# Kernel optimization log

Hardware: AMD Instinct MI355X
Metric: run time of the kernel (lower is better)

Reference implementation:

```python
import jax, jax.numpy as jnp
import numpy as np

SEQ, BATCH, D_MODEL = 1536, 2, 1024
N_HEAD, D_HEAD, N_ROLL = 16, 64, 3
SCALE = 1.0 / float(np.sqrt(D_HEAD))
EPS_DENOM = 1e-5
EPS_LN = 1e-5


def _dpfp(x, n_roll=N_ROLL):
    # relu feature map: cat(relu(x), relu(-x)), then roll-multiply expansion
    x = jnp.concatenate([jax.nn.relu(x), jax.nn.relu(-x)], axis=-1)  # [S,B,N,2D]
    return jnp.concatenate(
        [x * jnp.roll(x, shift=i, axis=-1) for i in range(1, n_roll + 1)], axis=-1
    )  # [S,B,N,2D*n_roll]


def setup_inputs() -> dict:
    key = jax.random.key(0)
    k_h, k_q, k_kv, k_o = jax.random.split(key, 4)
    std = 1.0 / float(np.sqrt(D_MODEL))
    h = jax.random.normal(k_h, (SEQ, BATCH, D_MODEL), jnp.float32)
    Wq = jax.random.normal(k_q, (N_HEAD * D_HEAD, D_MODEL), jnp.float32) * std
    Wkv = jax.random.normal(k_kv, (2 * N_HEAD * D_HEAD, D_MODEL), jnp.float32) * std
    Wo = jax.random.normal(k_o, (D_MODEL, N_HEAD * D_HEAD), jnp.float32) * std
    ln_gamma = jnp.ones((D_MODEL,), jnp.float32)
    ln_beta = jnp.zeros((D_MODEL,), jnp.float32)
    # Transformer-XL causal mask: triu(ones(qlen, klen), 1)[:, :, None] -> dim 3
    attn_mask = jnp.triu(jnp.ones((SEQ, SEQ), bool), k=1)[:, :, None]
    return {"h": h, "Wq": Wq, "Wkv": Wkv, "Wo": Wo,
            "ln_gamma": ln_gamma, "ln_beta": ln_beta, "attn_mask": attn_mask}


def reference(h, Wq, Wkv, Wo, ln_gamma, ln_beta, attn_mask):
    S, B, _ = h.shape
    # projections (no mems, post-lnorm, eval mode -> dropout identity)
    q = (h @ Wq.T).reshape(S, B, N_HEAD, D_HEAD)
    k, v = jnp.split(h @ Wkv.T, 2, axis=-1)
    k = k.reshape(S, B, N_HEAD, D_HEAD)
    v = v.reshape(S, B, N_HEAD, D_HEAD)
    # DPFP feature maps -> feature dim 2*D_HEAD*N_ROLL
    q = _dpfp(q)
    k = _dpfp(k)
    # kernelized scores [S,S,B,N]
    score = jnp.einsum('ibnd,jbnd->ijbn', q, k) * SCALE
    # 3-D mask [qlen,klen,1] -> broadcast over (b via size-1) and heads
    score = jnp.where(attn_mask[:, :, :, None], 0.0, score)
    # sum-normalization over keys (axis 1 = j)
    denom = jnp.sum(score, axis=1, keepdims=True) + EPS_DENOM
    prob = score / denom
    attn_vec = jnp.einsum('ijbn,jbnd->ibnd', prob, v).reshape(S, B, N_HEAD * D_HEAD)
    attn_out = attn_vec @ Wo.T
    # post-layernorm residual
    x = h + attn_out
    mean = jnp.mean(x, axis=-1, keepdims=True)
    var = jnp.var(x, axis=-1, keepdims=True)
    return ln_gamma * (x - mean) / jnp.sqrt(var + EPS_LN) + ln_beta
```

## Files before the change

### kernel.cpp

```cpp
#include <hip/hip_runtime.h>
#include <hip/hip_bf16.h>

#define S_LEN 1536
#define BATCH 2
#define DMODEL 1024
#define NHEAD 16
#define DHEAD 64
#define FDIM 384
#define CHUNK 64
#define NCHUNK 24
#define ROWS (S_LEN*BATCH)
#define SCALE_F 0.125f
#define EPS_D 1e-5f
#define EPS_LN 1e-5f

typedef unsigned short u16;
typedef __attribute__((ext_vector_type(8))) __bf16 bf16x8;
typedef __attribute__((ext_vector_type(8))) unsigned short ushort8;
typedef __attribute__((ext_vector_type(4))) float f32x4;

static __device__ __forceinline__ float bf2f(u16 a) {
  return __uint_as_float(((unsigned)a) << 16);
}
static __device__ __forceinline__ u16 f2bf(float x) {
  unsigned u = __float_as_uint(x);
  unsigned r = (u + 0x7FFFu + ((u >> 16) & 1u)) >> 16;
  return (u16)r;
}
static __device__ __forceinline__ void gload_lds16(const void* g, void* l) {
  __builtin_amdgcn_global_load_lds(
      (const __attribute__((address_space(1))) void*)g,
      (__attribute__((address_space(3))) void*)l, 16, 0, 0);
}
#define MFMA(a, b, c) __builtin_amdgcn_mfma_f32_16x16x32_bf16(a, b, c, 0, 0, 0)


__global__ __launch_bounds__(256) void cvt_bf16(
    const float* __restrict__ in, u16* __restrict__ out, int n4) {
  int i = blockIdx.x * 256 + threadIdx.x;
  if (i < n4) {
    float4 v = ((const float4*)in)[i];
    ushort4 o = {f2bf(v.x), f2bf(v.y), f2bf(v.z), f2bf(v.w)};
    ((ushort4*)out)[i] = o;
  }
}

__global__ __launch_bounds__(256) void gemm_bf16_mfma(
    const u16* __restrict__ A, const u16* __restrict__ B,
    float* __restrict__ C, int M, int N, int K) {
  __shared__ u16 As[128 * 32];
  __shared__ u16 Bs[128 * 32];
  const int t = threadIdx.x;
  const int l = t & 63, w = t >> 6;
  const int m0 = blockIdx.y * 128, n0 = blockIdx.x * 128;
  const int wm = (w >> 1) * 64, wn = (w & 1) * 64;

  f32x4 acc[4][4];
#pragma unroll
  for (int i = 0; i < 4; ++i)
#pragma unroll
    for (int j = 0; j < 4; ++j) acc[i][j] = (f32x4)0.f;

  const size_t Kb = (size_t)K * 2;
  const int o_lo = w * 1024 + l * 16;
  const int o_hi = 4096 + w * 1024 + l * 16;
  const int r_lo = o_lo >> 6, kb_lo = o_lo & 63;
  const int r_hi = o_hi >> 6, kb_hi = o_hi & 63;

  const char* Ap0 = (const char*)A + (size_t)(m0 + r_lo) * Kb + kb_lo;
  const char* Ap1 = (const char*)A + (size_t)(m0 + r_hi) * Kb + kb_hi;
  const char* Bp0 = (const char*)B + (size_t)(n0 + r_lo) * Kb + kb_lo;
  const char* Bp1 = (const char*)B + (size_t)(n0 + r_hi) * Kb + kb_hi;
  u16* AsB0 = As + (w * 1024) / 2;
  u16* AsB1 = As + (4096 + w * 1024) / 2;
  u16* BsB0 = Bs + (w * 1024) / 2;
  u16* BsB1 = Bs + (4096 + w * 1024) / 2;

  const int fr = l & 15, ko = (l >> 4) * 8;

  for (int k0 = 0; k0 < K; k0 += 32) {
    __syncthreads();
    gload_lds16(Ap0, AsB0);
    gload_lds16(Ap1, AsB1);
    gload_lds16(Bp0, BsB0);
    gload_lds16(Bp1, BsB1);
    Ap0 += 64; Ap1 += 64; Bp0 += 64; Bp1 += 64;
    __syncthreads();
    bf16x8 a[4], b[4];
#pragma unroll
    for (int m = 0; m < 4; ++m)
      a[m] = *(const bf16x8*)&As[(wm + m * 16 + fr) * 32 + ko];
#pragma unroll
    for (int n = 0; n < 4; ++n)
      b[n] = *(const bf16x8*)&Bs[(wn + n * 16 + fr) * 32 + ko];
#pragma unroll
    for (int m = 0; m < 4; ++m)
#pragma unroll
      for (int n = 0; n < 4; ++n)
        acc[m][n] = MFMA(a[m], b[n], acc[m][n]);
  }

  const int cr = (l >> 4) * 4, ccol = l & 15;
#pragma unroll
  for (int m = 0; m < 4; ++m)
#pragma unroll
    for (int n = 0; n < 4; ++n)
#pragma unroll
      for (int j = 0; j < 4; ++j)
        C[(size_t)(m0 + wm + m * 16 + cr + j) * N + (n0 + wn + n * 16 + ccol)] =
            acc[m][n][j];
}

__global__ __launch_bounds__(256) void gemm64_bf16(
    const u16* __restrict__ A, const u16* __restrict__ B,
    float* __restrict__ C, int M, int N, int K) {
  __shared__ u16 As[64 * 32];
  __shared__ u16 Bs[64 * 32];
  const int t = threadIdx.x;
  const int l = t & 63, w = t >> 6;
  const int m0 = blockIdx.y * 64, n0 = blockIdx.x * 64;
  const int fr = l & 15, kg = l >> 4;
  const size_t Kb = (size_t)K * 2;
  const int o = t * 16, r = o >> 6, kb = o & 63;
  const char* Ap = (const char*)A + (size_t)(m0 + r) * Kb + kb;
  const char* Bp = (const char*)B + (size_t)(n0 + r) * Kb + kb;
  u16* AsB = As + (w * 1024) / 2;
  u16* BsB = Bs + (w * 1024) / 2;
  f32x4 acc[4];
#pragma unroll
  for (int i = 0; i < 4; ++i) acc[i] = (f32x4)0.f;
  for (int k0 = 0; k0 < K; k0 += 32) {
    __syncthreads();
    gload_lds16(Ap, AsB);
    gload_lds16(Bp, BsB);
    Ap += 64; Bp += 64;
    __syncthreads();
    bf16x8 a = *(const bf16x8*)&As[(16 * w + fr) * 32 + kg * 8];
#pragma unroll
    for (int nt = 0; nt < 4; ++nt) {
      bf16x8 b = *(const bf16x8*)&Bs[(16 * nt + fr) * 32 + kg * 8];
      acc[nt] = MFMA(a, b, acc[nt]);
    }
  }
#pragma unroll
  for (int nt = 0; nt < 4; ++nt)
#pragma unroll
    for (int reg = 0; reg < 4; ++reg)
      C[(size_t)(m0 + 16 * w + 4 * kg + reg) * N + (n0 + 16 * nt + fr)] =
          acc[nt][reg];
}

__global__ __launch_bounds__(256) void dpfp_q64(
    const float* __restrict__ proj, u16* __restrict__ qft) {
  const int c = blockIdx.x, bn = blockIdx.y;
  const int b = bn >> 4, n = bn & 15;
  const int s0 = c * CHUNK;
  const int t = threadIdx.x;
  __shared__ float y[64][129];
  const int j = t >> 2, dq = (t & 3) << 4;
  const float* qp = proj + (size_t)((s0 + j) * BATCH + b) * 3072 + n * DHEAD + dq;
#pragma unroll
  for (int u = 0; u < 4; ++u) {
    float4 xv = *(const float4*)(qp + 4 * u);
    int d = dq + 4 * u;
    y[j][d + 0] = fmaxf(xv.x, 0.f); y[j][64 + d + 0] = fmaxf(-xv.x, 0.f);
    y[j][d + 1] = fmaxf(xv.y, 0.f); y[j][64 + d + 1] = fmaxf(-xv.y, 0.f);
    y[j][d + 2] = fmaxf(xv.z, 0.f); y[j][64 + d + 2] = fmaxf(-xv.z, 0.f);
    y[j][d + 3] = fmaxf(xv.w, 0.f); y[j][64 + d + 3] = fmaxf(-xv.w, 0.f);
  }
  __syncthreads();
  u16* base = qft + (size_t)bn * 589824;
  const int fr = t & 15, kg = (t >> 4) & 3, l = t & 63;
#pragma unroll 2
  for (int it = 0; it < 12; ++it) {
    int tile = it * 4 + (t >> 6);
    int rT = tile / 12, cB = tile % 12;
    int sl = rT * 16 + fr;
    ushort8 o;
#pragma unroll
    for (int e = 0; e < 8; ++e) {
      int f = cB * 32 + kg * 8 + e, m = f & 127, sh = (f >> 7) + 1;
      o[e] = f2bf(y[sl][m] * y[sl][(m - sh) & 127]);
    }
    *(ushort8*)(base + ((size_t)(4 * c + rT) * 12 + cB) * 512 + l * 8) = o;
  }
}

__global__ __launch_bounds__(256) void dpfp_k64(
    const float* __restrict__ proj, u16* __restrict__ kft,
    u16* __restrict__ kfTt, u16* __restrict__ vTt) {
  const int c = blockIdx.x, bn = blockIdx.y;
  const int b = bn >> 4, n = bn & 15;
  const int s0 = c * CHUNK;
  const int t = threadIdx.x;
  __shared__ float y[64][129];
  __shared__ float vs[64][65];
  const int j = t >> 2, dq = (t & 3) << 4;
  const float* kp = proj + (size_t)((s0 + j) * BATCH + b) * 3072 + n * DHEAD + dq;
#pragma unroll
  for (int u = 0; u < 4; ++u) {
    float4 xv = *(const float4*)(kp + 1024 + 4 * u);
    float4 vv = *(const float4*)(kp + 2048 + 4 * u);
    int d = dq + 4 * u;
    y[j][d + 0] = fmaxf(xv.x, 0.f); y[j][64 + d + 0] = fmaxf(-xv.x, 0.f);
    y[j][d + 1] = fmaxf(xv.y, 0.f); y[j][64 + d + 1] = fmaxf(-xv.y, 0.f);
    y[j][d + 2] = fmaxf(xv.z, 0.f); y[j][64 + d + 2] = fmaxf(-xv.z, 0.f);
    y[j][d + 3] = fmaxf(xv.w, 0.f); y[j][64 + d + 3] = fmaxf(-xv.w, 0.f);
    vs[j][d + 0] = vv.x; vs[j][d + 1] = vv.y;
    vs[j][d + 2] = vv.z; vs[j][d + 3] = vv.w;
  }
  __syncthreads();
  const int fr = t & 15, kg = (t >> 4) & 3, l = t & 63;
  {
    u16* base = kft + (size_t)bn * 589824;
#pragma unroll 2
    for (int it = 0; it < 12; ++it) {
      int tile = it * 4 + (t >> 6);
      int rT = tile / 12, cB = tile % 12;
      int sl = rT * 16 + fr;
      ushort8 o;
#pragma unroll
      for (int e = 0; e < 8; ++e) {
        int f = cB * 32 + kg * 8 + e, m = f & 127, sh = (f >> 7) + 1;
        o[e] = f2bf(y[sl][m] * y[sl][(m - sh) & 127]);
      }
      *(ushort8*)(base + ((size_t)(4 * c + rT) * 12 + cB) * 512 + l * 8) = o;
    }
  }
  {
    u16* base = kfTt + (size_t)bn * 589824;
#pragma unroll 2
    for (int it = 0; it < 12; ++it) {
      int tile = it * 4 + (t >> 6);
      int rT = tile >> 1, cHalf = tile & 1;
      int f = rT * 16 + fr, m = f & 127, sh = (f >> 7) + 1;
      int sb = cHalf * 32 + kg * 8;
      ushort8 o;
#pragma unroll
      for (int e = 0; e < 8; ++e)
        o[e] = f2bf(y[sb + e][m] * y[sb + e][(m - sh) & 127]);
      *(ushort8*)(base + ((size_t)rT * 48 + 2 * c + cHalf) * 512 + l * 8) = o;
    }
  }
  {
    u16* base = vTt + (size_t)bn * 98304;
#pragma unroll
    for (int it = 0; it < 2; ++it) {
      int tile = it * 4 + (t >> 6);
      int rT = tile >> 1, cHalf = tile & 1;
      int d = rT * 16 + fr;
      int sb = cHalf * 32 + kg * 8;
      ushort8 o;
#pragma unroll
      for (int e = 0; e < 8; ++e) o[e] = f2bf(vs[sb + e][d]);
      *(ushort8*)(base + ((size_t)rT * 48 + 2 * c + cHalf) * 512 + l * 8) = o;
    }
  }
}

__global__ __launch_bounds__(256) void chunk_kv_mfma(
    const u16* __restrict__ kfTt, const u16* __restrict__ vTt,
    u16* __restrict__ kvlin, float* __restrict__ ksumst) {
  const int c = blockIdx.x, bn = blockIdx.y;
  const int t = threadIdx.x, l = t & 63, w = t >> 6;
  const int fr = l & 15, kg = l >> 4;
  const u16* vt_base = vTt + (size_t)bn * 98304;
  const u16* kt_base = kfTt + (size_t)bn * 589824;

  f32x4 acc[4][6];
#pragma unroll
  for (int m = 0; m < 4; ++m)
#pragma unroll
    for (int nt = 0; nt < 6; ++nt) acc[m][nt] = (f32x4)0.f;
  float ks[6] = {0.f, 0.f, 0.f, 0.f, 0.f, 0.f};

#pragma unroll
  for (int ksi = 0; ksi < 2; ++ksi) {
    bf16x8 a[4];
#pragma unroll
    for (int m = 0; m < 4; ++m)
      a[m] = *(const bf16x8*)(vt_base + ((size_t)m * 48 + 2 * c + ksi) * 512 + l * 8);
#pragma unroll
    for (int nt = 0; nt < 6; ++nt) {
      const u16* bp = kt_base + ((size_t)(6 * w + nt) * 48 + 2 * c + ksi) * 512 + l * 8;
      bf16x8 bfrag = *(const bf16x8*)bp;
      ushort8 raw = *(const ushort8*)bp;
#pragma unroll
      for (int e = 0; e < 8; ++e) ks[nt] += bf2f(raw[e]);
#pragma unroll
      for (int m = 0; m < 4; ++m) acc[m][nt] = MFMA(a[m], bfrag, acc[m][nt]);
    }
  }
#pragma unroll
  for (int nt = 0; nt < 6; ++nt) {
    float x = ks[nt];
    x += __shfl_xor(x, 16);
    x += __shfl_xor(x, 32);
    ks[nt] = x;
  }
  if (l < 16) {
    float* kso = ksumst + (size_t)(bn * NCHUNK + c) * FDIM + 96 * w;
#pragma unroll
    for (int nt = 0; nt < 6; ++nt) kso[16 * nt + l] = ks[nt];
  }
  u16* outp = kvlin + (size_t)(bn * NCHUNK + c) * (64 * FDIM);
#pragma unroll
  for (int m = 0; m < 4; ++m)
#pragma unroll
    for (int nt = 0; nt < 6; ++nt)
#pragma unroll
      for (int reg = 0; reg < 4; ++reg) {
        int d = 16 * m + 4 * kg + reg, f = 96 * w + 16 * nt + fr;
        outp[(size_t)d * FDIM + f] = f2bf(acc[m][nt][reg]);
      }
}

__global__ __launch_bounds__(256) void scan_relayout(
    const u16* __restrict__ kvlin, float* __restrict__ ksumst,
    u16* __restrict__ kvswz) {
  const int bid = blockIdx.x;
  if (bid < 1536) {
    const int bn = bid / 48, rem = bid % 48, dT = rem / 12, cB = rem % 12;
    const int t = threadIdx.x;
    const int p = t * 2, l = p >> 3, e0 = p & 7;
    const int fr = l & 15, kg = l >> 4;
    const int d = dT * 16 + fr, f = cB * 32 + kg * 8 + e0;
    const u16* src = kvlin + (size_t)bn * (NCHUNK * 24576) + d * FDIM + f;
    float a0 = 0.f, a1 = 0.f;
    for (int c = 0; c < NCHUNK; ++c) {
      const u16* s2 = src + (size_t)c * 24576;
      float x0 = bf2f(s2[0]), x1 = bf2f(s2[1]);
      u16* dp = kvswz + (((size_t)(bn * NCHUNK + c) * 4 + dT) * 12 + cB) * 512 + l * 8 + e0;
      dp[0] = f2bf(a0); dp[1] = f2bf(a1);
      a0 += x0; a1 += x1;
    }
  } else {
    int gid = (bid - 1536) * 256 + threadIdx.x;
    int bn = gid / FDIM, f = gid % FDIM;
    float* base = ksumst + (size_t)bn * NCHUNK * FDIM + f;
    float a = 0.f;
    for (int c = 0; c < NCHUNK; ++c) {
      float x = base[(size_t)c * FDIM];
      base[(size_t)c * FDIM] = a;
      a += x;
    }
  }
}

__global__ __launch_bounds__(256) void attn_mfma(
    const u16* __restrict__ qft, const u16* __restrict__ kft,
    const u16* __restrict__ vTt, const u16* __restrict__ kvswz,
    const float* __restrict__ kspre, u16* __restrict__ attnvec) {
  const int c = blockIdx.x, bn = blockIdx.y;
  const int b = bn >> 4, n = bn & 15;
  const int s0 = c * CHUNK;
  const int t = threadIdx.x, l = t & 63, w = t >> 6;
  const int fr = l & 15, kg = l >> 4;

  const u16* qbase = qft + (size_t)bn * 589824;
  const u16* kbase = kft + (size_t)bn * 589824;
  const u16* vbase = vTt + (size_t)bn * 98304;
  const u16* kvbase = kvswz + (size_t)(bn * NCHUNK + c) * 24576;
  const float* ksp = kspre + (size_t)(bn * NCHUNK + c) * FDIM;

  __shared__ u16 Sb[64][70];

  f32x4 acc[9];
#pragma unroll
  for (int i = 0; i < 9; ++i) acc[i] = (f32x4)0.f;

#pragma unroll 3
  for (int cB = 0; cB < 12; ++cB) {
    bf16x8 a = *(const bf16x8*)(qbase + ((size_t)(4 * c + w) * 12 + cB) * 512 + l * 8);
#pragma unroll
    for (int nt = 0; nt < 4; ++nt) {
      bf16x8 bfrag = *(const bf16x8*)(kbase + ((size_t)(4 * c + nt) * 12 + cB) * 512 + l * 8);
      acc[nt] = MFMA(a, bfrag, acc[nt]);
    }
#pragma unroll
    for (int nt = 0; nt < 4; ++nt) {
      bf16x8 bfrag = *(const bf16x8*)(kvbase + ((size_t)nt * 12 + cB) * 512 + l * 8);
      acc[4 + nt] = MFMA(a, bfrag, acc[4 + nt]);
    }
    ushort8 bd = {0, 0, 0, 0, 0, 0, 0, 0};
    if (fr == 0) {
#pragma unroll
      for (int e = 0; e < 8; ++e) bd[e] = f2bf(ksp[cB * 32 + kg * 8 + e]);
    }
    union { ushort8 u; bf16x8 v; } cu;
    cu.u = bd;
    acc[8] = MFMA(a, cu.v, acc[8]);
  }

  float rsum[4];
#pragma unroll
  for (int reg = 0; reg < 4; ++reg) {
    int i = 16 * w + 4 * kg + reg;
    float r = 0.f;
#pragma unroll
    for (int nt = 0; nt < 4; ++nt) {
      int jj = 16 * nt + fr;
      float sval = (jj <= i) ? acc[nt][reg] : 0.f;
      acc[nt][reg] = sval;
      r += sval;
    }
    r += __shfl_xor(r, 1); r += __shfl_xor(r, 2);
    r += __shfl_xor(r, 4); r += __shfl_xor(r, 8);
    rsum[reg] = r;
  }
#pragma unroll
  for (int nt = 0; nt < 4; ++nt)
#pragma unroll
    for (int reg = 0; reg < 4; ++reg)
      Sb[16 * w + 4 * kg + reg][16 * nt + fr] = f2bf(acc[nt][reg]);

  __syncthreads();

#pragma unroll
  for (int ksi = 0; ksi < 2; ++ksi) {
    const int ko = ksi * 32 + kg * 8;
    bf16x8 a = *(const bf16x8*)&Sb[16 * w + fr][ko];
#pragma unroll
    for (int nt = 0; nt < 4; ++nt) {
      bf16x8 bfrag = *(const bf16x8*)(vbase + ((size_t)nt * 48 + 2 * c + ksi) * 512 + l * 8);
      acc[4 + nt] = MFMA(a, bfrag, acc[4 + nt]);
    }
  }

#pragma unroll
  for (int reg = 0; reg < 4; ++reg) {
    int i = 16 * w + 4 * kg + reg;
    float dinter = __shfl(acc[8][reg], l & 48);
    float den = rsum[reg] + dinter;
    float sc = SCALE_F / (SCALE_F * den + EPS_D);
    int rowg = (s0 + i) * BATCH + b;
    u16* orow = attnvec + (size_t)rowg * DMODEL + n * DHEAD;
#pragma unroll
    for (int nt = 0; nt < 4; ++nt)
      orow[16 * nt + fr] = f2bf(acc[4 + nt][reg] * sc);
  }
}

__global__ __launch_bounds__(256) void ln_kernel(
    const float* __restrict__ h, const float* __restrict__ ao,
    const float* __restrict__ gamma, const float* __restrict__ beta,
    float* __restrict__ out) {
  const int r = blockIdx.x, t = threadIdx.x;
  const float* hr = h + (size_t)r * DMODEL;
  const float* ar = ao + (size_t)r * DMODEL;
  float4 xh = *(const float4*)(hr + t * 4);
  float4 xa = *(const float4*)(ar + t * 4);
  float4 x = {xh.x + xa.x, xh.y + xa.y, xh.z + xa.z, xh.w + xa.w};
  float sum = x.x + x.y + x.z + x.w;
  float sq = x.x * x.x + x.y * x.y + x.z * x.z + x.w * x.w;
#pragma unroll
  for (int o = 32; o >= 1; o >>= 1) {
    sum += __shfl_xor(sum, o);
    sq += __shfl_xor(sq, o);
  }
  __shared__ float s_sum[4], s_sq[4];
  int w = t >> 6;
  if ((t & 63) == 0) { s_sum[w] = sum; s_sq[w] = sq; }
  __syncthreads();
  sum = s_sum[0] + s_sum[1] + s_sum[2] + s_sum[3];
  sq = s_sq[0] + s_sq[1] + s_sq[2] + s_sq[3];
  float mean = sum * (1.0f / DMODEL);
  float var = sq * (1.0f / DMODEL) - mean * mean;
  float rstd = rsqrtf(var + EPS_LN);
  float4 g = *(const float4*)(gamma + t * 4);
  float4 bb = *(const float4*)(beta + t * 4);
  float4 o4 = {g.x * (x.x - mean) * rstd + bb.x,
               g.y * (x.y - mean) * rstd + bb.y,
               g.z * (x.z - mean) * rstd + bb.z,
               g.w * (x.w - mean) * rstd + bb.w};
  *(float4*)(out + (size_t)r * DMODEL + t * 4) = o4;
}

extern "C" void kernel_launch(void* const* d_in, const int* in_sizes, int n_in,
                              void* d_out, int out_size, void* d_ws, size_t ws_size,
                              hipStream_t stream) {
  const float* h = (const float*)d_in[0];
  const float* Wq = (const float*)d_in[1];
  const float* Wkv = (const float*)d_in[2];
  const float* Wo = (const float*)d_in[3];
  const float* gamma = (const float*)d_in[4];
  const float* beta = (const float*)d_in[5];
  float* out = (float*)d_out;

  float* ws = (float*)d_ws;
  float* proj = ws;
  u16* qft = (u16*)(proj + 9437184);
  u16* kft = qft + 18874368;
  u16* kfTt = kft + 18874368;
  u16* vTt = kfTt + 18874368;
  u16* kvlin = vTt + 3145728;
  float* ksumst = (float*)(kvlin + 18874368);
  u16* Wo_bf = (u16*)(ksumst + 294912);
  u16* h_bf = kvlin;
  u16* Wqkv_bf = kvlin + 3145728;
  u16* kvswz = (u16*)proj;
  u16* attnvec = kvlin;
  float* attnout = (float*)kft;

  hipLaunchKernelGGL(cvt_bf16, dim3(3072), dim3(256), 0, stream, h, h_bf, 786432);
  hipLaunchKernelGGL(cvt_bf16, dim3(1024), dim3(256), 0, stream, Wq, Wqkv_bf, 262144);
  hipLaunchKernelGGL(cvt_bf16, dim3(2048), dim3(256), 0, stream,
                     Wkv, Wqkv_bf + 1048576, 524288);
  hipLaunchKernelGGL(cvt_bf16, dim3(1024), dim3(256), 0, stream, Wo, Wo_bf, 262144);

  hipLaunchKernelGGL(gemm_bf16_mfma, dim3(24, 24), dim3(256), 0, stream,
                     h_bf, Wqkv_bf, proj, ROWS, 3072, 1024);
  hipLaunchKernelGGL(dpfp_q64, dim3(24, 32), dim3(256), 0, stream, proj, qft);
  hipLaunchKernelGGL(dpfp_k64, dim3(24, 32), dim3(256), 0, stream,
                     proj, kft, kfTt, vTt);
  hipLaunchKernelGGL(chunk_kv_mfma, dim3(24, 32), dim3(256), 0, stream,
                     kfTt, vTt, kvlin, ksumst);
  hipLaunchKernelGGL(scan_relayout, dim3(1584), dim3(256), 0, stream,
                     kvlin, ksumst, kvswz);
  hipLaunchKernelGGL(attn_mfma, dim3(24, 32), dim3(256), 0, stream,
                     qft, kft, vTt, kvswz, ksumst, attnvec);
  hipLaunchKernelGGL(gemm64_bf16, dim3(16, 48), dim3(256), 0, stream,
                     attnvec, Wo_bf, attnout, ROWS, 1024, 1024);
  hipLaunchKernelGGL(ln_kernel, dim3(3072), dim3(256), 0, stream,
                     h, attnout, gamma, beta, out);
}
```

Measured before the change: 168.3 us.

## Fuse QKV projection GEMM with DPFP feature expansion and merge conversions

The four fp32-to-bf16 conversion launches become one kernel, and the QKV projection GEMM now writes its output tile to shared memory as bf16 and expands it directly into the DPFP Q/K/K-transposed/V-transposed tiled layouts. This removes the fp32 projection buffer round trip through global memory and two separate DPFP kernel launches. In exchange, the projection is rounded to bf16 before the relu/roll products, and the epilogue recomputes relu values per element with branchy shared-memory reads. Block work is also unbalanced: K blocks write two large outputs while V blocks write little.

```diff
diff --git a/kernel.cpp b/kernel.cpp
--- a/kernel.cpp
+++ b/kernel.cpp
@@ -35,24 +35,35 @@
 #define MFMA(a, b, c) __builtin_amdgcn_mfma_f32_16x16x32_bf16(a, b, c, 0, 0, 0)
 
 
-__global__ __launch_bounds__(256) void cvt_bf16(
-    const float* __restrict__ in, u16* __restrict__ out, int n4) {
+__global__ __launch_bounds__(256) void cvt_all(
+    const float* __restrict__ h, const float* __restrict__ Wq,
+    const float* __restrict__ Wkv, const float* __restrict__ Wo,
+    u16* __restrict__ h_bf, u16* __restrict__ Wqkv_bf, u16* __restrict__ Wo_bf) {
   int i = blockIdx.x * 256 + threadIdx.x;
-  if (i < n4) {
-    float4 v = ((const float4*)in)[i];
-    ushort4 o = {f2bf(v.x), f2bf(v.y), f2bf(v.z), f2bf(v.w)};
-    ((ushort4*)out)[i] = o;
-  }
-}
-
-__global__ __launch_bounds__(256) void gemm_bf16_mfma(
+  const float* src; u16* dst; int j;
+  if (i < 786432) { src = h; dst = h_bf; j = i; }
+  else if (i < 1048576) { src = Wq; dst = Wqkv_bf; j = i - 786432; }
+  else if (i < 1572864) { src = Wkv; dst = Wqkv_bf + 1048576; j = i - 1048576; }
+  else { src = Wo; dst = Wo_bf; j = i - 1572864; }
+  float4 v = ((const float4*)src)[j];
+  ushort4 o = {f2bf(v.x), f2bf(v.y), f2bf(v.z), f2bf(v.w)};
+  ((ushort4*)dst)[j] = o;
+}
+
+__global__ __launch_bounds__(256) void proj_dpfp(
     const u16* __restrict__ A, const u16* __restrict__ B,
-    float* __restrict__ C, int M, int N, int K) {
-  __shared__ u16 As[128 * 32];
-  __shared__ u16 Bs[128 * 32];
+    u16* __restrict__ qft, u16* __restrict__ kft,
+    u16* __restrict__ kfTt, u16* __restrict__ vTt) {
+  __shared__ __align__(16) char smem[33792];
+  u16* As = (u16*)smem;
+  u16* Bs = (u16*)(smem + 8192);
+  u16* Ysh = (u16*)smem;
+#define YSH(r, cc) Ysh[(r) * 132 + (cc)]
+
   const int t = threadIdx.x;
   const int l = t & 63, w = t >> 6;
-  const int m0 = blockIdx.y * 128, n0 = blockIdx.x * 128;
+  const int bx = blockIdx.x, c = blockIdx.y;
+  const int m0 = c * 128, n0 = bx * 128;
   const int wm = (w >> 1) * 64, wn = (w & 1) * 64;
 
   f32x4 acc[4][4];
@@ -61,7 +72,7 @@
 #pragma unroll
     for (int j = 0; j < 4; ++j) acc[i][j] = (f32x4)0.f;
 
-  const size_t Kb = (size_t)K * 2;
+  const size_t Kb = 2048;
   const int o_lo = w * 1024 + l * 16;
   const int o_hi = 4096 + w * 1024 + l * 16;
   const int r_lo = o_lo >> 6, kb_lo = o_lo & 63;
@@ -76,9 +87,10 @@
   u16* BsB0 = Bs + (w * 1024) / 2;
   u16* BsB1 = Bs + (4096 + w * 1024) / 2;
 
-  const int fr = l & 15, ko = (l >> 4) * 8;
-
-  for (int k0 = 0; k0 < K; k0 += 32) {
+  const int fr = l & 15, kg = l >> 4;
+  const int ko = kg * 8;
+
+  for (int k0 = 0; k0 < 1024; k0 += 32) {
     __syncthreads();
     gload_lds16(Ap0, AsB0);
     gload_lds16(Ap1, AsB1);
@@ -100,15 +112,97 @@
         acc[m][n] = MFMA(a[m], b[n], acc[m][n]);
   }
 
-  const int cr = (l >> 4) * 4, ccol = l & 15;
+  const int cr = kg * 4, ccol = fr;
+  __syncthreads();
 #pragma unroll
   for (int m = 0; m < 4; ++m)
 #pragma unroll
     for (int n = 0; n < 4; ++n)
 #pragma unroll
       for (int j = 0; j < 4; ++j)
-        C[(size_t)(m0 + wm + m * 16 + cr + j) * N + (n0 + wn + n * 16 + ccol)] =
-            acc[m][n][j];
+        YSH(wm + m * 16 + cr + j, wn + n * 16 + ccol) = f2bf(acc[m][n][j]);
+  __syncthreads();
+
+  if (bx < 8) {
+#pragma unroll
+    for (int tgt = 0; tgt < 4; ++tgt) {
+      const int hd = tgt & 1, b = tgt >> 1;
+      const int bn = b * 16 + bx * 2 + hd;
+      u16* base = qft + (size_t)bn * 589824;
+      for (int it = w; it < 48; it += 4) {
+        int rT = it / 12, cB = it % 12;
+        int row = 2 * (rT * 16 + fr) + b;
+        ushort8 o;
+#pragma unroll
+        for (int e = 0; e < 8; ++e) {
+          int f = cB * 32 + kg * 8 + e, m = f & 127, sh = (f >> 7) + 1, m2 = (m - sh) & 127;
+          float y1 = (m < 64) ? fmaxf(bf2f(YSH(row, hd * 64 + m)), 0.f)
+                              : fmaxf(-bf2f(YSH(row, hd * 64 + m - 64)), 0.f);
+          float y2 = (m2 < 64) ? fmaxf(bf2f(YSH(row, hd * 64 + m2)), 0.f)
+                               : fmaxf(-bf2f(YSH(row, hd * 64 + m2 - 64)), 0.f);
+          o[e] = f2bf(y1 * y2);
+        }
+        *(ushort8*)(base + ((size_t)(4 * c + rT) * 12 + cB) * 512 + l * 8) = o;
+      }
+    }
+  } else if (bx < 16) {
+    const int hx = bx - 8;
+#pragma unroll
+    for (int tgt = 0; tgt < 4; ++tgt) {
+      const int hd = tgt & 1, b = tgt >> 1;
+      const int bn = b * 16 + hx * 2 + hd;
+      u16* kbase = kft + (size_t)bn * 589824;
+      u16* ktbase = kfTt + (size_t)bn * 589824;
+      for (int it = w; it < 48; it += 4) {
+        int rT = it / 12, cB = it % 12;
+        int row = 2 * (rT * 16 + fr) + b;
+        ushort8 o;
+#pragma unroll
+        for (int e = 0; e < 8; ++e) {
+          int f = cB * 32 + kg * 8 + e, m = f & 127, sh = (f >> 7) + 1, m2 = (m - sh) & 127;
+          float y1 = (m < 64) ? fmaxf(bf2f(YSH(row, hd * 64 + m)), 0.f)
+                              : fmaxf(-bf2f(YSH(row, hd * 64 + m - 64)), 0.f);
+          float y2 = (m2 < 64) ? fmaxf(bf2f(YSH(row, hd * 64 + m2)), 0.f)
+                               : fmaxf(-bf2f(YSH(row, hd * 64 + m2 - 64)), 0.f);
+          o[e] = f2bf(y1 * y2);
+        }
+        *(ushort8*)(kbase + ((size_t)(4 * c + rT) * 12 + cB) * 512 + l * 8) = o;
+      }
+      for (int it = w; it < 48; it += 4) {
+        int rT = it >> 1, cHalf = it & 1;
+        int f = rT * 16 + fr, m = f & 127, sh = (f >> 7) + 1, m2 = (m - sh) & 127;
+        ushort8 o;
+#pragma unroll
+        for (int e = 0; e < 8; ++e) {
+          int row = 2 * (cHalf * 32 + kg * 8 + e) + b;
+          float y1 = (m < 64) ? fmaxf(bf2f(YSH(row, hd * 64 + m)), 0.f)
+                              : fmaxf(-bf2f(YSH(row, hd * 64 + m - 64)), 0.f);
+          float y2 = (m2 < 64) ? fmaxf(bf2f(YSH(row, hd * 64 + m2)), 0.f)
+                               : fmaxf(-bf2f(YSH(row, hd * 64 + m2 - 64)), 0.f);
+          o[e] = f2bf(y1 * y2);
+        }
+        *(ushort8*)(ktbase + ((size_t)rT * 48 + 2 * c + cHalf) * 512 + l * 8) = o;
+      }
+    }
+  } else {
+    const int hx = bx - 16;
+#pragma unroll
+    for (int tgt = 0; tgt < 4; ++tgt) {
+      const int hd = tgt & 1, b = tgt >> 1;
+      const int bn = b * 16 + hx * 2 + hd;
+      u16* vbase = vTt + (size_t)bn * 98304;
+      for (int it = w; it < 8; it += 4) {
+        int rT = it >> 1, cHalf = it & 1;
+        int d = rT * 16 + fr;
+        ushort8 o;
+#pragma unroll
+        for (int e = 0; e < 8; ++e)
+          o[e] = YSH(2 * (cHalf * 32 + kg * 8 + e) + b, hd * 64 + d);
+        *(ushort8*)(vbase + ((size_t)rT * 48 + 2 * c + cHalf) * 512 + l * 8) = o;
+      }
+    }
+  }
+#undef YSH
 }
 
 __global__ __launch_bounds__(256) void gemm64_bf16(
@@ -148,114 +242,6 @@
     for (int reg = 0; reg < 4; ++reg)
       C[(size_t)(m0 + 16 * w + 4 * kg + reg) * N + (n0 + 16 * nt + fr)] =
           acc[nt][reg];
-}
-
-__global__ __launch_bounds__(256) void dpfp_q64(
-    const float* __restrict__ proj, u16* __restrict__ qft) {
-  const int c = blockIdx.x, bn = blockIdx.y;
-  const int b = bn >> 4, n = bn & 15;
-  const int s0 = c * CHUNK;
-  const int t = threadIdx.x;
-  __shared__ float y[64][129];
-  const int j = t >> 2, dq = (t & 3) << 4;
-  const float* qp = proj + (size_t)((s0 + j) * BATCH + b) * 3072 + n * DHEAD + dq;
-#pragma unroll
-  for (int u = 0; u < 4; ++u) {
-    float4 xv = *(const float4*)(qp + 4 * u);
-    int d = dq + 4 * u;
-    y[j][d + 0] = fmaxf(xv.x, 0.f); y[j][64 + d + 0] = fmaxf(-xv.x, 0.f);
-    y[j][d + 1] = fmaxf(xv.y, 0.f); y[j][64 + d + 1] = fmaxf(-xv.y, 0.f);
-    y[j][d + 2] = fmaxf(xv.z, 0.f); y[j][64 + d + 2] = fmaxf(-xv.z, 0.f);
-    y[j][d + 3] = fmaxf(xv.w, 0.f); y[j][64 + d + 3] = fmaxf(-xv.w, 0.f);
-  }
-  __syncthreads();
-  u16* base = qft + (size_t)bn * 589824;
-  const int fr = t & 15, kg = (t >> 4) & 3, l = t & 63;
-#pragma unroll 2
-  for (int it = 0; it < 12; ++it) {
-    int tile = it * 4 + (t >> 6);
-    int rT = tile / 12, cB = tile % 12;
-    int sl = rT * 16 + fr;
-    ushort8 o;
-#pragma unroll
-    for (int e = 0; e < 8; ++e) {
-      int f = cB * 32 + kg * 8 + e, m = f & 127, sh = (f >> 7) + 1;
-      o[e] = f2bf(y[sl][m] * y[sl][(m - sh) & 127]);
-    }
-    *(ushort8*)(base + ((size_t)(4 * c + rT) * 12 + cB) * 512 + l * 8) = o;
-  }
-}
-
-__global__ __launch_bounds__(256) void dpfp_k64(
-    const float* __restrict__ proj, u16* __restrict__ kft,
-    u16* __restrict__ kfTt, u16* __restrict__ vTt) {
-  const int c = blockIdx.x, bn = blockIdx.y;
-  const int b = bn >> 4, n = bn & 15;
-  const int s0 = c * CHUNK;
-  const int t = threadIdx.x;
-  __shared__ float y[64][129];
-  __shared__ float vs[64][65];
-  const int j = t >> 2, dq = (t & 3) << 4;
-  const float* kp = proj + (size_t)((s0 + j) * BATCH + b) * 3072 + n * DHEAD + dq;
-#pragma unroll
-  for (int u = 0; u < 4; ++u) {
-    float4 xv = *(const float4*)(kp + 1024 + 4 * u);
-    float4 vv = *(const float4*)(kp + 2048 + 4 * u);
-    int d = dq + 4 * u;
-    y[j][d + 0] = fmaxf(xv.x, 0.f); y[j][64 + d + 0] = fmaxf(-xv.x, 0.f);
-    y[j][d + 1] = fmaxf(xv.y, 0.f); y[j][64 + d + 1] = fmaxf(-xv.y, 0.f);
-    y[j][d + 2] = fmaxf(xv.z, 0.f); y[j][64 + d + 2] = fmaxf(-xv.z, 0.f);
-    y[j][d + 3] = fmaxf(xv.w, 0.f); y[j][64 + d + 3] = fmaxf(-xv.w, 0.f);
-    vs[j][d + 0] = vv.x; vs[j][d + 1] = vv.y;
-    vs[j][d + 2] = vv.z; vs[j][d + 3] = vv.w;
-  }
-  __syncthreads();
-  const int fr = t & 15, kg = (t >> 4) & 3, l = t & 63;
-  {
-    u16* base = kft + (size_t)bn * 589824;
-#pragma unroll 2
-    for (int it = 0; it < 12; ++it) {
-      int tile = it * 4 + (t >> 6);
-      int rT = tile / 12, cB = tile % 12;
-      int sl = rT * 16 + fr;
-      ushort8 o;
-#pragma unroll
-      for (int e = 0; e < 8; ++e) {
-        int f = cB * 32 + kg * 8 + e, m = f & 127, sh = (f >> 7) + 1;
-        o[e] = f2bf(y[sl][m] * y[sl][(m - sh) & 127]);
-      }
-      *(ushort8*)(base + ((size_t)(4 * c + rT) * 12 + cB) * 512 + l * 8) = o;
-    }
-  }
-  {
-    u16* base = kfTt + (size_t)bn * 589824;
-#pragma unroll 2
-    for (int it = 0; it < 12; ++it) {
-      int tile = it * 4 + (t >> 6);
-      int rT = tile >> 1, cHalf = tile & 1;
-      int f = rT * 16 + fr, m = f & 127, sh = (f >> 7) + 1;
-      int sb = cHalf * 32 + kg * 8;
-      ushort8 o;
-#pragma unroll
-      for (int e = 0; e < 8; ++e)
-        o[e] = f2bf(y[sb + e][m] * y[sb + e][(m - sh) & 127]);
-      *(ushort8*)(base + ((size_t)rT * 48 + 2 * c + cHalf) * 512 + l * 8) = o;
-    }
-  }
-  {
-    u16* base = vTt + (size_t)bn * 98304;
-#pragma unroll
-    for (int it = 0; it < 2; ++it) {
-      int tile = it * 4 + (t >> 6);
-      int rT = tile >> 1, cHalf = tile & 1;
-      int d = rT * 16 + fr;
-      int sb = cHalf * 32 + kg * 8;
-      ushort8 o;
-#pragma unroll
-      for (int e = 0; e < 8; ++e) o[e] = f2bf(vs[sb + e][d]);
-      *(ushort8*)(base + ((size_t)rT * 48 + 2 * c + cHalf) * 512 + l * 8) = o;
-    }
-  }
 }
 
 __global__ __launch_bounds__(256) void chunk_kv_mfma(
@@ -488,31 +474,23 @@
   float* out = (float*)d_out;
 
   float* ws = (float*)d_ws;
-  float* proj = ws;
-  u16* qft = (u16*)(proj + 9437184);
+  u16* qft = (u16*)ws;
   u16* kft = qft + 18874368;
   u16* kfTt = kft + 18874368;
   u16* vTt = kfTt + 18874368;
   u16* kvlin = vTt + 3145728;
-  float* ksumst = (float*)(kvlin + 18874368);
+  u16* kvswz = kvlin + 18874368;
+  float* ksumst = (float*)(kvswz + 18874368);
   u16* Wo_bf = (u16*)(ksumst + 294912);
   u16* h_bf = kvlin;
   u16* Wqkv_bf = kvlin + 3145728;
-  u16* kvswz = (u16*)proj;
   u16* attnvec = kvlin;
-  float* attnout = (float*)kft;
-
-  hipLaunchKernelGGL(cvt_bf16, dim3(3072), dim3(256), 0, stream, h, h_bf, 786432);
-  hipLaunchKernelGGL(cvt_bf16, dim3(1024), dim3(256), 0, stream, Wq, Wqkv_bf, 262144);
-  hipLaunchKernelGGL(cvt_bf16, dim3(2048), dim3(256), 0, stream,
-                     Wkv, Wqkv_bf + 1048576, 524288);
-  hipLaunchKernelGGL(cvt_bf16, dim3(1024), dim3(256), 0, stream, Wo, Wo_bf, 262144);
-
-  hipLaunchKernelGGL(gemm_bf16_mfma, dim3(24, 24), dim3(256), 0, stream,
-                     h_bf, Wqkv_bf, proj, ROWS, 3072, 1024);
-  hipLaunchKernelGGL(dpfp_q64, dim3(24, 32), dim3(256), 0, stream, proj, qft);
-  hipLaunchKernelGGL(dpfp_k64, dim3(24, 32), dim3(256), 0, stream,
-                     proj, kft, kfTt, vTt);
+  float* attnout = (float*)kfTt;
+
+  hipLaunchKernelGGL(cvt_all, dim3(7168), dim3(256), 0, stream,
+                     h, Wq, Wkv, Wo, h_bf, Wqkv_bf, Wo_bf);
+  hipLaunchKernelGGL(proj_dpfp, dim3(24, 24), dim3(256), 0, stream,
+                     h_bf, Wqkv_bf, qft, kft, kfTt, vTt);
   hipLaunchKernelGGL(chunk_kv_mfma, dim3(24, 32), dim3(256), 0, stream,
                      kfTt, vTt, kvlin, ksumst);
   hipLaunchKernelGGL(scan_relayout, dim3(1584), dim3(256), 0, stream,
```

New measurement: 232.2 us. +37.9%, slower.

## Fuse chunk KV products with prefix scan; merge conversions; swizzle GEMM block order

Applied to the files above, without the earlier changes.

Replaces the per-chunk KV outer-product kernel and the separate scan/relayout kernel with a single kernel. Each block owns one (batch-head, feature tile) and walks the chunks sequentially, keeping the running prefix in registers and writing the exclusive-scan result directly in swizzled layout. This removes the round trip of the bf16 kvlin intermediate through global memory and drops a launch. The four bf16 conversion launches become one. Both GEMMs remap block IDs in an XCD-style interleave to improve L2 locality. The cost is that the fused kernel has a serial dependence over 24 chunks with only 384 blocks, which may limit parallelism.

```diff
diff --git a/kernel.cpp b/kernel.cpp
--- a/kernel.cpp
+++ b/kernel.cpp
@@ -35,14 +35,19 @@
 #define MFMA(a, b, c) __builtin_amdgcn_mfma_f32_16x16x32_bf16(a, b, c, 0, 0, 0)
 
 
-__global__ __launch_bounds__(256) void cvt_bf16(
-    const float* __restrict__ in, u16* __restrict__ out, int n4) {
+__global__ __launch_bounds__(256) void cvt_all(
+    const float* __restrict__ h, const float* __restrict__ Wq,
+    const float* __restrict__ Wkv, const float* __restrict__ Wo,
+    u16* __restrict__ h_bf, u16* __restrict__ Wqkv_bf, u16* __restrict__ Wo_bf) {
   int i = blockIdx.x * 256 + threadIdx.x;
-  if (i < n4) {
-    float4 v = ((const float4*)in)[i];
-    ushort4 o = {f2bf(v.x), f2bf(v.y), f2bf(v.z), f2bf(v.w)};
-    ((ushort4*)out)[i] = o;
-  }
+  const float* src; u16* dst; int j;
+  if (i < 786432) { src = h; dst = h_bf; j = i; }
+  else if (i < 1048576) { src = Wq; dst = Wqkv_bf; j = i - 786432; }
+  else if (i < 1572864) { src = Wkv; dst = Wqkv_bf + 1048576; j = i - 1048576; }
+  else { src = Wo; dst = Wo_bf; j = i - 1572864; }
+  float4 v = ((const float4*)src)[j];
+  ushort4 o = {f2bf(v.x), f2bf(v.y), f2bf(v.z), f2bf(v.w)};
+  ((ushort4*)dst)[j] = o;
 }
 
 __global__ __launch_bounds__(256) void gemm_bf16_mfma(
@@ -52,7 +57,11 @@
   __shared__ u16 Bs[128 * 32];
   const int t = threadIdx.x;
   const int l = t & 63, w = t >> 6;
-  const int m0 = blockIdx.y * 128, n0 = blockIdx.x * 128;
+  const int nbx = gridDim.x;
+  const int fl = blockIdx.y * nbx + blockIdx.x;
+  const int q8 = (nbx * gridDim.y) >> 3;
+  const int fl2 = (fl & 7) * q8 + (fl >> 3);
+  const int m0 = (fl2 / nbx) * 128, n0 = (fl2 % nbx) * 128;
   const int wm = (w >> 1) * 64, wn = (w & 1) * 64;
 
   f32x4 acc[4][4];
@@ -118,7 +127,11 @@
   __shared__ u16 Bs[64 * 32];
   const int t = threadIdx.x;
   const int l = t & 63, w = t >> 6;
-  const int m0 = blockIdx.y * 64, n0 = blockIdx.x * 64;
+  const int nbx = gridDim.x;
+  const int fl = blockIdx.y * nbx + blockIdx.x;
+  const int q8 = (nbx * gridDim.y) >> 3;
+  const int fl2 = (fl & 7) * q8 + (fl >> 3);
+  const int m0 = (fl2 / nbx) * 64, n0 = (fl2 % nbx) * 64;
   const int fr = l & 15, kg = l >> 4;
   const size_t Kb = (size_t)K * 2;
   const int o = t * 16, r = o >> 6, kb = o & 63;
@@ -258,92 +271,66 @@
   }
 }
 
-__global__ __launch_bounds__(256) void chunk_kv_mfma(
+__global__ __launch_bounds__(256) void chunk_kv_scan(
     const u16* __restrict__ kfTt, const u16* __restrict__ vTt,
-    u16* __restrict__ kvlin, float* __restrict__ ksumst) {
-  const int c = blockIdx.x, bn = blockIdx.y;
+    u16* __restrict__ kvswz, float* __restrict__ ksumst) {
+  const int fl = blockIdx.x;
+  const int fl2 = (fl & 7) * 48 + (fl >> 3);
+  const int bn = fl2 / 12, ft2 = fl2 % 12;
   const int t = threadIdx.x, l = t & 63, w = t >> 6;
   const int fr = l & 15, kg = l >> 4;
   const u16* vt_base = vTt + (size_t)bn * 98304;
   const u16* kt_base = kfTt + (size_t)bn * 589824;
 
-  f32x4 acc[4][6];
-#pragma unroll
-  for (int m = 0; m < 4; ++m)
-#pragma unroll
-    for (int nt = 0; nt < 6; ++nt) acc[m][nt] = (f32x4)0.f;
-  float ks[6] = {0.f, 0.f, 0.f, 0.f, 0.f, 0.f};
-
-#pragma unroll
-  for (int ksi = 0; ksi < 2; ++ksi) {
-    bf16x8 a[4];
-#pragma unroll
-    for (int m = 0; m < 4; ++m)
-      a[m] = *(const bf16x8*)(vt_base + ((size_t)m * 48 + 2 * c + ksi) * 512 + l * 8);
-#pragma unroll
-    for (int nt = 0; nt < 6; ++nt) {
-      const u16* bp = kt_base + ((size_t)(6 * w + nt) * 48 + 2 * c + ksi) * 512 + l * 8;
-      bf16x8 bfrag = *(const bf16x8*)bp;
-      ushort8 raw = *(const ushort8*)bp;
-#pragma unroll
-      for (int e = 0; e < 8; ++e) ks[nt] += bf2f(raw[e]);
-#pragma unroll
-      for (int m = 0; m < 4; ++m) acc[m][nt] = MFMA(a[m], bfrag, acc[m][nt]);
-    }
-  }
-#pragma unroll
-  for (int nt = 0; nt < 6; ++nt) {
-    float x = ks[nt];
-    x += __shfl_xor(x, 16);
-    x += __shfl_xor(x, 32);
-    ks[nt] = x;
-  }
-  if (l < 16) {
-    float* kso = ksumst + (size_t)(bn * NCHUNK + c) * FDIM + 96 * w;
-#pragma unroll
-    for (int nt = 0; nt < 6; ++nt) kso[16 * nt + l] = ks[nt];
-  }
-  u16* outp = kvlin + (size_t)(bn * NCHUNK + c) * (64 * FDIM);
-#pragma unroll
-  for (int m = 0; m < 4; ++m)
-#pragma unroll
-    for (int nt = 0; nt < 6; ++nt)
-#pragma unroll
-      for (int reg = 0; reg < 4; ++reg) {
-        int d = 16 * m + 4 * kg + reg, f = 96 * w + 16 * nt + fr;
-        outp[(size_t)d * FDIM + f] = f2bf(acc[m][nt][reg]);
+  __shared__ u16 Ys[64][40];
+
+  f32x4 pacc0 = (f32x4)0.f, pacc1 = (f32x4)0.f;
+  float pks = 0.f;
+
+  for (int c = 0; c < NCHUNK; ++c) {
+    f32x4 acc0 = (f32x4)0.f, acc1 = (f32x4)0.f;
+    float ksp = 0.f;
+#pragma unroll
+    for (int ksi = 0; ksi < 2; ++ksi) {
+      bf16x8 a = *(const bf16x8*)(vt_base + ((size_t)w * 48 + 2 * c + ksi) * 512 + l * 8);
+      const u16* bp0 = kt_base + ((size_t)(2 * ft2 + 0) * 48 + 2 * c + ksi) * 512 + l * 8;
+      const u16* bp1 = kt_base + ((size_t)(2 * ft2 + 1) * 48 + 2 * c + ksi) * 512 + l * 8;
+      bf16x8 b0 = *(const bf16x8*)bp0;
+      bf16x8 b1 = *(const bf16x8*)bp1;
+      if (w == 0) {
+        ushort8 raw = *(const ushort8*)bp0;
+#pragma unroll
+        for (int e = 0; e < 8; ++e) ksp += bf2f(raw[e]);
+      } else if (w == 1) {
+        ushort8 raw = *(const ushort8*)bp1;
+#pragma unroll
+        for (int e = 0; e < 8; ++e) ksp += bf2f(raw[e]);
       }
-}
-
-__global__ __launch_bounds__(256) void scan_relayout(
-    const u16* __restrict__ kvlin, float* __restrict__ ksumst,
-    u16* __restrict__ kvswz) {
-  const int bid = blockIdx.x;
-  if (bid < 1536) {
-    const int bn = bid / 48, rem = bid % 48, dT = rem / 12, cB = rem % 12;
-    const int t = threadIdx.x;
-    const int p = t * 2, l = p >> 3, e0 = p & 7;
-    const int fr = l & 15, kg = l >> 4;
-    const int d = dT * 16 + fr, f = cB * 32 + kg * 8 + e0;
-    const u16* src = kvlin + (size_t)bn * (NCHUNK * 24576) + d * FDIM + f;
-    float a0 = 0.f, a1 = 0.f;
-    for (int c = 0; c < NCHUNK; ++c) {
-      const u16* s2 = src + (size_t)c * 24576;
-      float x0 = bf2f(s2[0]), x1 = bf2f(s2[1]);
-      u16* dp = kvswz + (((size_t)(bn * NCHUNK + c) * 4 + dT) * 12 + cB) * 512 + l * 8 + e0;
-      dp[0] = f2bf(a0); dp[1] = f2bf(a1);
-      a0 += x0; a1 += x1;
-    }
-  } else {
-    int gid = (bid - 1536) * 256 + threadIdx.x;
-    int bn = gid / FDIM, f = gid % FDIM;
-    float* base = ksumst + (size_t)bn * NCHUNK * FDIM + f;
-    float a = 0.f;
-    for (int c = 0; c < NCHUNK; ++c) {
-      float x = base[(size_t)c * FDIM];
-      base[(size_t)c * FDIM] = a;
-      a += x;
-    }
+      acc0 = MFMA(a, b0, acc0);
+      acc1 = MFMA(a, b1, acc1);
+    }
+    __syncthreads();
+#pragma unroll
+    for (int reg = 0; reg < 4; ++reg) {
+      Ys[16 * w + 4 * kg + reg][fr] = f2bf(pacc0[reg]);
+      Ys[16 * w + 4 * kg + reg][16 + fr] = f2bf(pacc1[reg]);
+    }
+    __syncthreads();
+    {
+      ushort8 o = *(const ushort8*)&Ys[w * 16 + fr][kg * 8];
+      *(ushort8*)(kvswz + (size_t)(bn * NCHUNK + c) * 24576 +
+                  (size_t)(w * 12 + ft2) * 512 + l * 8) = o;
+    }
+    if (w < 2) {
+      float x = ksp;
+      x += __shfl_xor(x, 16);
+      x += __shfl_xor(x, 32);
+      if (kg == 0)
+        ksumst[(size_t)(bn * NCHUNK + c) * FDIM + ft2 * 32 + w * 16 + fr] = pks;
+      pks += x;
+    }
+    pacc0 += acc0;
+    pacc1 += acc1;
   }
 }
 
@@ -493,30 +480,23 @@
   u16* kft = qft + 18874368;
   u16* kfTt = kft + 18874368;
   u16* vTt = kfTt + 18874368;
-  u16* kvlin = vTt + 3145728;
-  float* ksumst = (float*)(kvlin + 18874368);
+  u16* kvswz = vTt + 3145728;
+  float* ksumst = (float*)(kvswz + 18874368);
   u16* Wo_bf = (u16*)(ksumst + 294912);
-  u16* h_bf = kvlin;
-  u16* Wqkv_bf = kvlin + 3145728;
-  u16* kvswz = (u16*)proj;
-  u16* attnvec = kvlin;
-  float* attnout = (float*)kft;
-
-  hipLaunchKernelGGL(cvt_bf16, dim3(3072), dim3(256), 0, stream, h, h_bf, 786432);
-  hipLaunchKernelGGL(cvt_bf16, dim3(1024), dim3(256), 0, stream, Wq, Wqkv_bf, 262144);
-  hipLaunchKernelGGL(cvt_bf16, dim3(2048), dim3(256), 0, stream,
-                     Wkv, Wqkv_bf + 1048576, 524288);
-  hipLaunchKernelGGL(cvt_bf16, dim3(1024), dim3(256), 0, stream, Wo, Wo_bf, 262144);
-
+  u16* h_bf = kvswz;
+  u16* Wqkv_bf = kvswz + 3145728;
+  u16* attnvec = (u16*)proj;
+  float* attnout = proj + 1572864;
+
+  hipLaunchKernelGGL(cvt_all, dim3(7168), dim3(256), 0, stream,
+                     h, Wq, Wkv, Wo, h_bf, Wqkv_bf, Wo_bf);
   hipLaunchKernelGGL(gemm_bf16_mfma, dim3(24, 24), dim3(256), 0, stream,
                      h_bf, Wqkv_bf, proj, ROWS, 3072, 1024);
   hipLaunchKernelGGL(dpfp_q64, dim3(24, 32), dim3(256), 0, stream, proj, qft);
   hipLaunchKernelGGL(dpfp_k64, dim3(24, 32), dim3(256), 0, stream,
                      proj, kft, kfTt, vTt);
-  hipLaunchKernelGGL(chunk_kv_mfma, dim3(24, 32), dim3(256), 0, stream,
-                     kfTt, vTt, kvlin, ksumst);
-  hipLaunchKernelGGL(scan_relayout, dim3(1584), dim3(256), 0, stream,
-                     kvlin, ksumst, kvswz);
+  hipLaunchKernelGGL(chunk_kv_scan, dim3(384), dim3(256), 0, stream,
+                     kfTt, vTt, kvswz, ksumst);
   hipLaunchKernelGGL(attn_mfma, dim3(24, 32), dim3(256), 0, stream,
                      qft, kft, vTt, kvswz, ksumst, attnvec);
   hipLaunchKernelGGL(gemm64_bf16, dim3(16, 48), dim3(256), 0, stream,
```

New measurement: 152.2 us. 9.6% less time.
